# Kernel optimization log

Measured on AMD Instinct MI355X. Metric: run time of the kernel, lower is better.

Reference implementation:

```python
import jax, jax.numpy as jnp
import numpy as np

V = 6890      # SMPL vertex count
JNT = 24      # SMPL joints
NB = 10       # shape betas
PF = 207      # pose-blend features = 23*9
NJ_OUT = 19   # cocoplus joints
PARENTS = np.array([0, 0, 0, 0, 1, 2, 3, 4, 5, 6, 7, 8, 9, 9, 9, 12, 13, 14, 16, 17, 18, 19, 20, 21], dtype=np.int32)


def setup_inputs() -> dict:
    key = jax.random.key(0)
    ks = jax.random.split(key, 8)
    B = 512
    beta = jax.random.normal(ks[0], (B, NB), dtype=jnp.float32)
    theta = jax.random.normal(ks[1], (B, JNT * 3), dtype=jnp.float32)
    v_template = jax.random.normal(ks[2], (V, 3), dtype=jnp.float32)
    shapedirs = jax.random.normal(ks[3], (NB, V * 3), dtype=jnp.float32) * 0.01
    J_regressor = jax.random.uniform(ks[4], (V, JNT), dtype=jnp.float32)
    J_regressor = J_regressor / jnp.sum(J_regressor, axis=0, keepdims=True)
    posedirs = jax.random.normal(ks[5], (PF, V * 3), dtype=jnp.float32) * 0.01
    lbs_weights = jax.random.uniform(ks[6], (V, JNT), dtype=jnp.float32)
    lbs_weights = lbs_weights / jnp.sum(lbs_weights, axis=1, keepdims=True)
    joint_regressor = jax.random.uniform(ks[7], (V, NJ_OUT), dtype=jnp.float32)
    joint_regressor = joint_regressor / jnp.sum(joint_regressor, axis=0, keepdims=True)
    return {
        "beta": beta, "theta": theta, "v_template": v_template,
        "shapedirs": shapedirs, "J_regressor": J_regressor,
        "posedirs": posedirs, "lbs_weights": lbs_weights,
        "joint_regressor": joint_regressor,
    }


def batch_rodrigues(aa):
    # aa: [N,3] axis-angle -> [N,3,3] rotation via unit quaternion
    angle = jnp.linalg.norm(aa + 1e-8, axis=1, keepdims=True)  # [N,1]
    axis = aa / angle
    half = angle * 0.5
    w = jnp.cos(half)[:, 0]
    xyz = axis * jnp.sin(half)
    x, y, z = xyz[:, 0], xyz[:, 1], xyz[:, 2]
    w2, x2, y2, z2 = w * w, x * x, y * y, z * z
    wx, wy, wz = w * x, w * y, w * z
    xy, xz, yz = x * y, x * z, y * z
    R = jnp.stack([
        w2 + x2 - y2 - z2, 2 * (xy - wz), 2 * (xz + wy),
        2 * (xy + wz), w2 - x2 + y2 - z2, 2 * (yz - wx),
        2 * (xz - wy), 2 * (yz + wx), w2 - x2 - y2 + z2,
    ], axis=1).reshape(-1, 3, 3)
    return R


def _make_A(R, t):
    # R: [B,3,3], t: [B,3] -> [B,4,4]
    B = R.shape[0]
    top = jnp.concatenate([R, t[:, :, None]], axis=2)          # [B,3,4]
    bot = jnp.broadcast_to(jnp.array([0., 0., 0., 1.], R.dtype), (B, 1, 4))
    return jnp.concatenate([top, bot], axis=1)


def global_rigid_transform(Rs, J):
    # Rs: [B,24,3,3], J: [B,24,3]; kinematic-chain FK
    results = [_make_A(Rs[:, 0], J[:, 0])]
    for i in range(1, JNT):
        t = J[:, i] - J[:, PARENTS[i]]
        results.append(results[PARENTS[i]] @ _make_A(Rs[:, i], t))
    A = jnp.stack(results, axis=1)                              # [B,24,4,4]
    J_transformed = A[:, :, :3, 3]
    # remove rest-pose joint translation: A - [0 | A @ [J;0]]
    J_homo = jnp.concatenate([J, jnp.zeros_like(J[:, :, :1])], axis=2)  # [B,24,4]
    init_bone = jnp.einsum('bjpq,bjq->bjp', A, J_homo)          # [B,24,4]
    A_rel = A - jnp.concatenate(
        [jnp.zeros(A.shape[:3] + (3,), A.dtype), init_bone[..., None]], axis=-1)
    return J_transformed, A_rel


def reference(beta, theta, v_template, shapedirs, J_regressor, posedirs,
              lbs_weights, joint_regressor):
    B = beta.shape[0]
    # shape blend
    v_shaped = (beta @ shapedirs).reshape(B, V, 3) + v_template   # [B,V,3]
    # rest-pose joints
    J = jnp.einsum('bvc,vj->bjc', v_shaped, J_regressor)          # [B,24,3]
    # pose rotations
    Rs = batch_rodrigues(theta.reshape(-1, 3)).reshape(B, JNT, 3, 3)
    pose_feature = (Rs[:, 1:] - jnp.eye(3, dtype=Rs.dtype)).reshape(B, PF)
    v_posed = (pose_feature @ posedirs).reshape(B, V, 3) + v_shaped
    # FK
    _, A = global_rigid_transform(Rs, J)                          # [B,24,4,4]
    # skinning
    T = jnp.einsum('vj,bjpq->bvpq', lbs_weights, A)               # [B,V,4,4]
    v_homo = jnp.concatenate(
        [v_posed, jnp.ones((B, V, 1), v_posed.dtype)], axis=2)    # [B,V,4]
    verts = jnp.einsum('bvpq,bvq->bvp', T[:, :, :3, :], v_homo)   # [B,V,3]
    joints = jnp.einsum('bvc,vj->bjc', verts, joint_regressor)    # [B,19,3]
    return joints
```

## Files before the change

### kernel.cpp

```cpp
#include <hip/hip_runtime.h>
#include <math.h>

#define NV 6890
#define N3 20670
#define NJNT 24
#define NBETA 10
#define NPF 207
#define NJO 19
#define NBATCH 512
#define NJK 456
#define NJKP 512
#define NCOEF 218
#define PROWSP 768
#define KPAD 6912
#define KSPLIT 12
#define KCH 576
#define CSTR 224
#define CSTRV 6912

#define TR2 54
#define RODB 48
#define SJB 264
#define PMA 5913
#define PMO 27
#define PMZ 3051
#define PMT (PMA + PMO + PMZ)
#define CHB 48
#define C4R 1728
#define CMB (NJKP * C4R / 256)
#define D4R 219
#define RSP 2
#define RCH 109
#define SSTRIDE ((size_t)NBATCH * 3 * NJK)

typedef __attribute__((ext_vector_type(8))) short bfx8;
typedef __attribute__((ext_vector_type(4))) float fx4;

#define LDSP(x) ((__attribute__((address_space(3))) void*)(x))
#define GLBP(x) ((const __attribute__((address_space(1))) void*)(x))

__constant__ int d_par[NJNT] = {0,0,0,0,1,2,3,4,5,6,7,8,9,9,9,12,13,14,16,17,18,19,20,21};
__constant__ int d_path[NJNT][9] = {
  {0,-1,-1,-1,-1,-1,-1,-1,-1},
  {0,1,-1,-1,-1,-1,-1,-1,-1},
  {0,2,-1,-1,-1,-1,-1,-1,-1},
  {0,3,-1,-1,-1,-1,-1,-1,-1},
  {0,1,4,-1,-1,-1,-1,-1,-1},
  {0,2,5,-1,-1,-1,-1,-1,-1},
  {0,3,6,-1,-1,-1,-1,-1,-1},
  {0,1,4,7,-1,-1,-1,-1,-1},
  {0,2,5,8,-1,-1,-1,-1,-1},
  {0,3,6,9,-1,-1,-1,-1,-1},
  {0,1,4,7,10,-1,-1,-1,-1},
  {0,2,5,8,11,-1,-1,-1,-1},
  {0,3,6,9,12,-1,-1,-1,-1},
  {0,3,6,9,13,-1,-1,-1,-1},
  {0,3,6,9,14,-1,-1,-1,-1},
  {0,3,6,9,12,15,-1,-1,-1},
  {0,3,6,9,13,16,-1,-1,-1},
  {0,3,6,9,14,17,-1,-1,-1},
  {0,3,6,9,13,16,18,-1,-1},
  {0,3,6,9,14,17,19,-1,-1},
  {0,3,6,9,13,16,18,20,-1},
  {0,3,6,9,14,17,19,21,-1},
  {0,3,6,9,13,16,18,20,22},
  {0,3,6,9,14,17,19,21,23}};

__device__ inline short f2bf(float f) {
  union { float f; unsigned u; } x; x.f = f;
  unsigned r = (x.u + 0x7fffu + ((x.u >> 16) & 1u)) >> 16;
  return (short)r;
}

__global__ void __launch_bounds__(256) kA(const float* __restrict__ jr,
                                          const float* __restrict__ lbs,
                                          const float* __restrict__ Jreg,
                                          const float* __restrict__ sdirs,
                                          const float* __restrict__ vtmpl,
                                          const float* __restrict__ theta,
                                          const float* __restrict__ beta,
                                          const float* __restrict__ pdirs,
                                          float* __restrict__ jrT, float* __restrict__ wT,
                                          float* __restrict__ SJ, float* __restrict__ Rs,
                                          float* __restrict__ pfc,
                                          short* __restrict__ Pb) {
  __shared__ float red[4][3];
  __shared__ float tj[128 * NJO];
  __shared__ float tw[128 * NJNT];
  int bx = blockIdx.x, tid = threadIdx.x;
  if (bx < TR2) {
    int v0 = bx * 128;
    for (int i = tid; i < 128 * NJO; i += 256) {
      int g = v0 * NJO + i;
      tj[i] = (g < NV * NJO) ? jr[g] : 0.f;
    }
    for (int i = tid; i < 128 * NJNT; i += 256) {
      int g = v0 * NJNT + i;
      tw[i] = (g < NV * NJNT) ? lbs[g] : 0.f;
    }
    __syncthreads();
    for (int i = tid; i < 128 * (NJO + NJNT); i += 256) {
      int r = i >> 7, c = i & 127;
      int v = v0 + c;
      if (v >= NV) continue;
      if (r < NJO) jrT[(size_t)r * CSTRV + v] = tj[c * NJO + r];
      else         wT[(size_t)(r - NJO) * CSTRV + v] = tw[c * NJNT + (r - NJO)];
    }
  } else if (bx < TR2 + RODB) {
    int t2 = (bx - TR2) * 256 + tid;
    int b = t2 / NJNT, j = t2 - b * NJNT;
    float a0 = theta[b * 72 + j * 3 + 0];
    float a1 = theta[b * 72 + j * 3 + 1];
    float a2 = theta[b * 72 + j * 3 + 2];
    float e0 = a0 + 1e-8f, e1 = a1 + 1e-8f, e2 = a2 + 1e-8f;
    float ang = sqrtf(e0 * e0 + e1 * e1 + e2 * e2);
    float inv = 1.0f / ang;
    float h = 0.5f * ang;
    float w = cosf(h), s = sinf(h);
    float x = a0 * inv * s, y = a1 * inv * s, z = a2 * inv * s;
    float R[9];
    R[0] = w*w + x*x - y*y - z*z; R[1] = 2.f*(x*y - w*z); R[2] = 2.f*(x*z + w*y);
    R[3] = 2.f*(x*y + w*z); R[4] = w*w - x*x + y*y - z*z; R[5] = 2.f*(y*z - w*x);
    R[6] = 2.f*(x*z - w*y); R[7] = 2.f*(y*z + w*x); R[8] = w*w - x*x - y*y + z*z;
#pragma unroll
    for (int r = 0; r < 9; ++r) Rs[b * 216 + j * 9 + r] = R[r];
    if (j >= 1) {
#pragma unroll
      for (int r = 0; r < 9; ++r)
        pfc[b * CSTR + (j - 1) * 9 + r] = R[r] - ((r % 4 == 0) ? 1.0f : 0.0f);
    } else {
#pragma unroll
      for (int i = 0; i < NBETA; ++i) pfc[b * CSTR + NPF + i] = beta[b * NBETA + i];
      pfc[b * CSTR + NPF + NBETA] = 1.0f;
    }
  } else if (bx < TR2 + RODB + SJB) {
    int s = bx - TR2 - RODB;
    int j = s % NJNT, k = s / NJNT;
    const float* src = (k < NBETA) ? (sdirs + (size_t)k * N3) : vtmpl;
    float a0 = 0.f, a1 = 0.f, a2 = 0.f;
    for (int v = tid; v < NV; v += 256) {
      float w = Jreg[v * NJNT + j];
      a0 += w * src[v * 3 + 0];
      a1 += w * src[v * 3 + 1];
      a2 += w * src[v * 3 + 2];
    }
    int lane = tid & 63, wid = tid >> 6;
#pragma unroll
    for (int s2 = 1; s2 < 64; s2 <<= 1) {
      a0 += __shfl_xor(a0, s2); a1 += __shfl_xor(a1, s2); a2 += __shfl_xor(a2, s2);
    }
    if (lane == 0) { red[wid][0] = a0; red[wid][1] = a1; red[wid][2] = a2; }
    __syncthreads();
    if (tid == 0) {
      float* o = SJ + (k * NJNT + j) * 3;
      o[0] = red[0][0] + red[1][0] + red[2][0] + red[3][0];
      o[1] = red[0][1] + red[1][1] + red[2][1] + red[3][1];
      o[2] = red[0][2] + red[1][2] + red[2][2] + red[3][2];
    }
  } else {
    int s4 = bx - TR2 - RODB - SJB;
    if (s4 < PMA) {
      int s = s4 / 27, g = s4 - s * 27;
      const float* src; int base;
      if (s < 207)      { src = pdirs + (size_t)s * N3;         base = 3 * s; }
      else if (s < 217) { src = sdirs + (size_t)(s - 207) * N3; base = 621 + 3 * (s - 207); }
      else              { src = vtmpl;                           base = 651; }
      int v = g * 256 + tid;
      float x = 0.f, y = 0.f, z = 0.f;
      if (v < NV) { x = src[3 * v]; y = src[3 * v + 1]; z = src[3 * v + 2]; }
      Pb[(size_t)(base + 0) * KPAD + v] = f2bf(x);
      Pb[(size_t)(base + 1) * KPAD + v] = f2bf(y);
      Pb[(size_t)(base + 2) * KPAD + v] = f2bf(z);
    } else if (s4 < PMA + PMO) {
      int g = s4 - PMA;
      int v = g * 256 + tid;
      Pb[(size_t)654 * KPAD + v] = (v < NV) ? f2bf(1.0f) : (short)0;
    } else {
      int s = s4 - PMA - PMO;
      int row = 655 + s / 27, g = s % 27;
      Pb[(size_t)row * KPAD + g * 256 + tid] = (short)0;
    }
  }
}

__device__ inline void getJ(const float* __restrict__ SJ, const float* bb, int i,
                            float& o0, float& o1, float& o2) {
  int r = i * 3;
  float a0 = SJ[NBETA * 72 + r + 0];
  float a1 = SJ[NBETA * 72 + r + 1];
  float a2 = SJ[NBETA * 72 + r + 2];
#pragma unroll
  for (int k = 0; k < NBETA; ++k) {
    a0 += bb[k] * SJ[k * 72 + r + 0];
    a1 += bb[k] * SJ[k * 72 + r + 1];
    a2 += bb[k] * SJ[k * 72 + r + 2];
  }
  o0 = a0; o1 = a1; o2 = a2;
}

__global__ void __launch_bounds__(256) kB(const float* __restrict__ beta,
                                          const float* __restrict__ SJ,
                                          const float* __restrict__ Rs,
                                          const float* __restrict__ jrT,
                                          const float* __restrict__ wT,
                                          float* __restrict__ A,
                                          short* __restrict__ Cb) {
  int bx = blockIdx.x, tid = threadIdx.x;
  if (bx < CHB) {
    int idx = bx * 256 + tid;
    int b = idx / NJNT, j = idx - b * NJNT;
    const float* Rb = Rs + b * 216;
    float bb[NBETA];
#pragma unroll
    for (int k = 0; k < NBETA; ++k) bb[k] = beta[b * NBETA + k];
    float jp0, jp1, jp2;
    getJ(SJ, bb, 0, jp0, jp1, jp2);
    float T[12];
#pragma unroll
    for (int r = 0; r < 3; ++r) {
      T[r * 4 + 0] = Rb[r * 3 + 0];
      T[r * 4 + 1] = Rb[r * 3 + 1];
      T[r * 4 + 2] = Rb[r * 3 + 2];
    }
    T[3] = jp0; T[7] = jp1; T[11] = jp2;
    for (int d = 1; d < 9; ++d) {
      int i = d_path[j][d];
      if (i < 0) break;
      float ji0, ji1, ji2;
      getJ(SJ, bb, i, ji0, ji1, ji2);
      float t0 = ji0 - jp0, t1 = ji1 - jp1, t2 = ji2 - jp2;
      const float* R = Rb + i * 9;
      float R0 = R[0], R1 = R[1], R2 = R[2], R3 = R[3], R4 = R[4];
      float R5 = R[5], R6 = R[6], R7 = R[7], R8 = R[8];
#pragma unroll
      for (int r = 0; r < 3; ++r) {
        float a0 = T[r * 4 + 0], a1 = T[r * 4 + 1], a2 = T[r * 4 + 2];
        T[r * 4 + 0] = a0 * R0 + a1 * R3 + a2 * R6;
        T[r * 4 + 1] = a0 * R1 + a1 * R4 + a2 * R7;
        T[r * 4 + 2] = a0 * R2 + a1 * R5 + a2 * R8;
        T[r * 4 + 3] = a0 * t0 + a1 * t1 + a2 * t2 + T[r * 4 + 3];
      }
      jp0 = ji0; jp1 = ji1; jp2 = ji2;
    }
    float* Ab = A + b * 288 + j * 12;
#pragma unroll
    for (int r = 0; r < 3; ++r) {
      float o0 = T[r * 4 + 0], o1 = T[r * 4 + 1], o2 = T[r * 4 + 2];
      Ab[r * 4 + 0] = o0;
      Ab[r * 4 + 1] = o1;
      Ab[r * 4 + 2] = o2;
      Ab[r * 4 + 3] = T[r * 4 + 3] - (o0 * jp0 + o1 * jp1 + o2 * jp2);
    }
  } else {
    int idx = (bx - CHB) * 256 + tid;
    int jk = idx / C4R;
    int c4 = idx - jk * C4R;
    int v0 = c4 * 4;
    short4 o;
    if (jk < NJK) {
      int j = jk / NJNT, k = jk - j * NJNT;
      float4 a = *(const float4*)(jrT + (size_t)j * CSTRV + v0);
      float4 w = *(const float4*)(wT + (size_t)k * CSTRV + v0);
      o.x = (v0 + 0 < NV) ? f2bf(a.x * w.x) : (short)0;
      o.y = (v0 + 1 < NV) ? f2bf(a.y * w.y) : (short)0;
      o.z = (v0 + 2 < NV) ? f2bf(a.z * w.z) : (short)0;
      o.w = (v0 + 3 < NV) ? f2bf(a.w * w.w) : (short)0;
    } else {
      o.x = o.y = o.z = o.w = (short)0;
    }
    *(short4*)(Cb + (size_t)jk * KPAD + v0) = o;
  }
}

__global__ void __launch_bounds__(256) k_gemm(const short* __restrict__ Pb,
                                              const short* __restrict__ Cb,
                                              float* __restrict__ Dpart) {
  int m0 = blockIdx.x * 128;
  int n0 = blockIdx.y * 64;
  int kb0 = blockIdx.z * KCH;
  __shared__ __align__(16) short As[128 * 64];
  __shared__ __align__(16) short Bs[64 * 64];
  int t = threadIdx.x;
  int wid = t >> 6, lane = t & 63;
  int fgrp = lane >> 4;
  fx4 acc[2][4];
#pragma unroll
  for (int r2 = 0; r2 < 2; ++r2)
#pragma unroll
    for (int j = 0; j < 4; ++j)
#pragma unroll
      for (int r = 0; r < 4; ++r) acc[r2][j][r] = 0.f;

  int lrow = lane >> 3;
  int gsrc = (lane & 7) ^ lrow;
  const short* sA[4]; short* dA[4];
#pragma unroll
  for (int i = 0; i < 4; ++i) {
    int rb = wid * 8 + i * 32;
    sA[i] = Pb + (size_t)(m0 + rb + lrow) * KPAD + kb0 + gsrc * 8;
    dA[i] = As + rb * 64;
  }
  const short* sB[2]; short* dB[2];
#pragma unroll
  for (int i = 0; i < 2; ++i) {
    int rb = wid * 8 + i * 32;
    sB[i] = Cb + (size_t)(n0 + rb + lrow) * KPAD + kb0 + gsrc * 8;
    dB[i] = Bs + rb * 64;
  }

  for (int kk = 0; kk < KCH / 64; ++kk) {
#pragma unroll
    for (int i = 0; i < 4; ++i) {
      __builtin_amdgcn_global_load_lds(GLBP(sA[i]), LDSP(dA[i]), 16, 0, 0);
      sA[i] += 64;
    }
#pragma unroll
    for (int i = 0; i < 2; ++i) {
      __builtin_amdgcn_global_load_lds(GLBP(sB[i]), LDSP(dB[i]), 16, 0, 0);
      sB[i] += 64;
    }
    __syncthreads();
#pragma unroll
    for (int ks = 0; ks < 2; ++ks) {
      int ga = ks * 4 + fgrp;
#pragma unroll
      for (int r2 = 0; r2 < 2; ++r2) {
        int arow = wid * 32 + r2 * 16 + (lane & 15);
        bfx8 a = *(const bfx8*)(As + arow * 64 + (ga ^ (arow & 7)) * 8);
#pragma unroll
        for (int j = 0; j < 4; ++j) {
          int bcol = j * 16 + (lane & 15);
          bfx8 b = *(const bfx8*)(Bs + bcol * 64 + (ga ^ (bcol & 7)) * 8);
          acc[r2][j] = __builtin_amdgcn_mfma_f32_16x16x32_bf16(a, b, acc[r2][j], 0, 0, 0);
        }
      }
    }
    __syncthreads();
  }
  float* dz = Dpart + (size_t)blockIdx.z * PROWSP * NJKP;
#pragma unroll
  for (int r2 = 0; r2 < 2; ++r2) {
    float* dst = dz + (size_t)(m0 + wid * 32 + r2 * 16 + (lane >> 4) * 4) * NJKP
               + n0 + (lane & 15);
#pragma unroll
    for (int j = 0; j < 4; ++j)
#pragma unroll
      for (int r = 0; r < 4; ++r)
        dst[(size_t)r * NJKP + j * 16] = acc[r2][j][r];
  }
}

__global__ void k_redD4(const float* __restrict__ Dpart, float* __restrict__ D4) {
  int idx = blockIdx.x * 256 + threadIdx.x;
  if (idx >= D4R * NJKP) return;
  int r = idx / NJKP, jk = idx - r * NJKP;
  float4 o;
  if (r < NCOEF) {
    float s0 = 0.f, s1 = 0.f, s2 = 0.f;
#pragma unroll
    for (int z = 0; z < KSPLIT; ++z) {
      const float* dp = Dpart + (size_t)z * PROWSP * NJKP + jk;
      s0 += dp[(size_t)(3 * r + 0) * NJKP];
      s1 += dp[(size_t)(3 * r + 1) * NJKP];
      s2 += dp[(size_t)(3 * r + 2) * NJKP];
    }
    o = make_float4(s0, s1, s2, 0.f);
  } else {
    float s = 0.f;
#pragma unroll
    for (int z = 0; z < KSPLIT; ++z)
      s += Dpart[(size_t)z * PROWSP * NJKP + (size_t)654 * NJKP + jk];
    o = make_float4(s, 0.f, 0.f, 0.f);
  }
  ((float4*)D4)[idx] = o;
}

__global__ void __launch_bounds__(256) k_S5b(const float* __restrict__ D4,
                                             const float* __restrict__ pfc,
                                             float* __restrict__ Spart) {
  int n0 = blockIdx.x * 64;
  int b0 = blockIdx.y * 8;
  int r0 = blockIdx.z * RCH;
  int r1 = r0 + RCH; if (r1 > NCOEF) r1 = NCOEF;
  int tid = threadIdx.x;
  int jk = tid & 63;
  int bg = (tid >> 6) * 2;
  const float4* D4v = (const float4*)D4;
  int jkg = n0 + jk;
  const float* c0p = pfc + (size_t)(b0 + bg + 0) * CSTR;
  const float* c1p = pfc + (size_t)(b0 + bg + 1) * CSTR;
  float a00 = 0.f, a01 = 0.f, a02 = 0.f, a10 = 0.f, a11 = 0.f, a12 = 0.f;
#pragma unroll 4
  for (int r = r0; r < r1; ++r) {
    float4 d = D4v[(size_t)r * NJKP + jkg];
    float c0 = c0p[r];
    float c1 = c1p[r];
    a00 += c0 * d.x; a01 += c0 * d.y; a02 += c0 * d.z;
    a10 += c1 * d.x; a11 += c1 * d.y; a12 += c1 * d.z;
  }
  if (jkg < NJK) {
    float* base = Spart + (size_t)blockIdx.z * SSTRIDE;
    float* o0 = base + ((size_t)(b0 + bg + 0) * 3) * NJK + jkg;
    float* o1 = base + ((size_t)(b0 + bg + 1) * 3) * NJK + jkg;
    o0[0 * NJK] = a00; o0[1 * NJK] = a01; o0[2 * NJK] = a02;
    o1[0 * NJK] = a10; o1[1 * NJK] = a11; o1[2 * NJK] = a12;
  }
}

__global__ void __launch_bounds__(128) k_final3(const float* __restrict__ Spart,
                                                const float* __restrict__ D4,
                                                const float* __restrict__ A,
                                                float* __restrict__ out) {
  __shared__ float S_ls[2 * 3 * NJK];
  __shared__ float A_ls[2 * 288];
  __shared__ float c0_ls[NJK];
  int blk = blockIdx.x, tid = threadIdx.x;
  int b0 = blk * 2;
  size_t sbase = (size_t)(b0 * 3) * NJK;
  for (int i = tid; i < 2 * 3 * NJK; i += 128)
    S_ls[i] = Spart[sbase + i] + Spart[SSTRIDE + sbase + i];
  for (int i = tid; i < 2 * 288; i += 128)
    A_ls[i] = A[(size_t)b0 * 288 + i];
  for (int i = tid; i < NJK; i += 128)
    c0_ls[i] = D4[((size_t)NCOEF * NJKP + i) * 4];
  __syncthreads();
  if (tid >= 2 * NJO * 3) return;
  int bq = tid / 57, r = tid - bq * 57;
  int j = r / 3, c = r - j * 3;
  const float* S0 = S_ls + (bq * 3 + 0) * NJK + j * NJNT;
  const float* S1 = S_ls + (bq * 3 + 1) * NJK + j * NJNT;
  const float* S2 = S_ls + (bq * 3 + 2) * NJK + j * NJNT;
  const float* Ab = A_ls + bq * 288;
  const float* cc = c0_ls + j * NJNT;
  float acc = 0.f;
#pragma unroll 4
  for (int k = 0; k < NJNT; ++k) {
    const float* Ar = Ab + k * 12 + c * 4;
    acc += Ar[0] * S0[k] + Ar[1] * S1[k] + Ar[2] * S2[k] + Ar[3] * cc[k];
  }
  out[(size_t)(b0 + bq) * 57 + r] = acc;
}

extern "C" void kernel_launch(void* const* d_in, const int* in_sizes, int n_in,
                              void* d_out, int out_size, void* d_ws, size_t ws_size,
                              hipStream_t stream) {
  const float* beta  = (const float*)d_in[0];
  const float* theta = (const float*)d_in[1];
  const float* vtmpl = (const float*)d_in[2];
  const float* sdirs = (const float*)d_in[3];
  const float* Jreg  = (const float*)d_in[4];
  const float* pdirs = (const float*)d_in[5];
  const float* lbs   = (const float*)d_in[6];
  const float* jreg2 = (const float*)d_in[7];
  float* out = (float*)d_out;

  float* ws    = (float*)d_ws;
  short* Cb    = (short*)ws;
  short* Pb    = Cb + (size_t)NJKP * KPAD;
  float* Dpart = (float*)(Pb + (size_t)PROWSP * KPAD);
  float* D4    = Dpart + (size_t)KSPLIT * PROWSP * NJKP;
  float* Spart = D4    + (size_t)D4R * NJKP * 4;
  float* pfc   = Spart + (size_t)RSP * SSTRIDE;
  float* Rs    = pfc   + (size_t)NBATCH * CSTR;
  float* A     = Rs    + (size_t)NBATCH * 216;
  float* jrT   = A     + (size_t)NBATCH * 288;
  float* wT    = jrT   + (size_t)NJO * CSTRV;
  float* SJ    = wT    + (size_t)NJNT * CSTRV;

  kA<<<dim3(TR2 + RODB + SJB + PMT), 256, 0, stream>>>(
      jreg2, lbs, Jreg, sdirs, vtmpl, theta, beta, pdirs,
      jrT, wT, SJ, Rs, pfc, Pb);
  kB<<<dim3(CHB + CMB), 256, 0, stream>>>(beta, SJ, Rs, jrT, wT, A, Cb);
  k_gemm<<<dim3(PROWSP / 128, NJKP / 64, KSPLIT), 256, 0, stream>>>(Pb, Cb, Dpart);
  k_redD4<<<dim3((D4R * NJKP + 255) / 256), 256, 0, stream>>>(Dpart, D4);
  k_S5b<<<dim3(NJKP / 64, NBATCH / 8, RSP), 256, 0, stream>>>(D4, pfc, Spart);
  k_final3<<<dim3(NBATCH / 2), 128, 0, stream>>>(Spart, D4, A, out);
}
```

Measured before the change: 79.43 us.

## Rebalance setup kernels, vectorize Pb packing, move FK into reduction kernel

The packing of posedirs/shapedirs/template into bf16 now uses float4 loads and short4 stores, with one thread handling four vertices, and zero-fill is done with short4 stores. The shape-joint regression moves from kA to kB and reads a transposed J_regressor, which kA now also writes, so the accesses are coalesced. The forward-kinematics chain moves from kB into the split-K reduction kernel, since it needs SJ from kB. The GEMM K-split drops from 12 to 9 slices with larger chunks, which means less partial-sum traffic and fewer blocks. Together these rebalance work across the launches and shorten the long serial blocks.

```diff
diff --git a/kernel.cpp b/kernel.cpp
--- a/kernel.cpp
+++ b/kernel.cpp
@@ -13,21 +13,20 @@
 #define NCOEF 218
 #define PROWSP 768
 #define KPAD 6912
-#define KSPLIT 12
-#define KCH 576
+#define KSPLIT 9
+#define KCH 768
 #define CSTR 224
 #define CSTRV 6912
 
 #define TR2 54
 #define RODB 48
-#define SJB 264
-#define PMA 5913
-#define PMO 27
-#define PMZ 3051
-#define PMT (PMA + PMO + PMZ)
-#define CHB 48
+#define PMV 1479
+#define PMP 763
 #define C4R 1728
 #define CMB (NJKP * C4R / 256)
+#define SJB 264
+#define RD4B 438
+#define CHB 48
 #define D4R 219
 #define RSP 2
 #define RCH 109
@@ -81,12 +80,12 @@
                                           const float* __restrict__ beta,
                                           const float* __restrict__ pdirs,
                                           float* __restrict__ jrT, float* __restrict__ wT,
-                                          float* __restrict__ SJ, float* __restrict__ Rs,
-                                          float* __restrict__ pfc,
+                                          float* __restrict__ jgT,
+                                          float* __restrict__ Rs, float* __restrict__ pfc,
                                           short* __restrict__ Pb) {
-  __shared__ float red[4][3];
   __shared__ float tj[128 * NJO];
   __shared__ float tw[128 * NJNT];
+  __shared__ float tg[128 * NJNT];
   int bx = blockIdx.x, tid = threadIdx.x;
   if (bx < TR2) {
     int v0 = bx * 128;
@@ -97,14 +96,16 @@
     for (int i = tid; i < 128 * NJNT; i += 256) {
       int g = v0 * NJNT + i;
       tw[i] = (g < NV * NJNT) ? lbs[g] : 0.f;
+      tg[i] = (g < NV * NJNT) ? Jreg[g] : 0.f;
     }
     __syncthreads();
-    for (int i = tid; i < 128 * (NJO + NJNT); i += 256) {
+    for (int i = tid; i < 128 * (NJO + 2 * NJNT); i += 256) {
       int r = i >> 7, c = i & 127;
       int v = v0 + c;
       if (v >= NV) continue;
-      if (r < NJO) jrT[(size_t)r * CSTRV + v] = tj[c * NJO + r];
-      else         wT[(size_t)(r - NJO) * CSTRV + v] = tw[c * NJNT + (r - NJO)];
+      if (r < NJO)            jrT[(size_t)r * CSTRV + v] = tj[c * NJO + r];
+      else if (r < NJO + NJNT) wT[(size_t)(r - NJO) * CSTRV + v] = tw[c * NJNT + (r - NJO)];
+      else                    jgT[(size_t)(r - NJO - NJNT) * CSTRV + v] = tg[c * NJNT + (r - NJO - NJNT)];
     }
   } else if (bx < TR2 + RODB) {
     int t2 = (bx - TR2) * 256 + tid;
@@ -133,126 +134,66 @@
       for (int i = 0; i < NBETA; ++i) pfc[b * CSTR + NPF + i] = beta[b * NBETA + i];
       pfc[b * CSTR + NPF + NBETA] = 1.0f;
     }
-  } else if (bx < TR2 + RODB + SJB) {
-    int s = bx - TR2 - RODB;
-    int j = s % NJNT, k = s / NJNT;
-    const float* src = (k < NBETA) ? (sdirs + (size_t)k * N3) : vtmpl;
-    float a0 = 0.f, a1 = 0.f, a2 = 0.f;
-    for (int v = tid; v < NV; v += 256) {
-      float w = Jreg[v * NJNT + j];
-      a0 += w * src[v * 3 + 0];
-      a1 += w * src[v * 3 + 1];
-      a2 += w * src[v * 3 + 2];
-    }
-    int lane = tid & 63, wid = tid >> 6;
-#pragma unroll
-    for (int s2 = 1; s2 < 64; s2 <<= 1) {
-      a0 += __shfl_xor(a0, s2); a1 += __shfl_xor(a1, s2); a2 += __shfl_xor(a2, s2);
-    }
-    if (lane == 0) { red[wid][0] = a0; red[wid][1] = a1; red[wid][2] = a2; }
-    __syncthreads();
-    if (tid == 0) {
-      float* o = SJ + (k * NJNT + j) * 3;
-      o[0] = red[0][0] + red[1][0] + red[2][0] + red[3][0];
-      o[1] = red[0][1] + red[1][1] + red[2][1] + red[3][1];
-      o[2] = red[0][2] + red[1][2] + red[2][2] + red[3][2];
+  } else if (bx < TR2 + RODB + PMV) {
+    int idx = (bx - TR2 - RODB) * 256 + tid;
+    if (idx >= 219 * C4R) return;
+    int s = idx / C4R, c4 = idx - s * C4R;
+    int v0 = c4 * 4;
+    if (s == 218) {
+      short one = f2bf(1.0f);
+      short4 o;
+      o.x = (v0 + 0 < NV) ? one : (short)0;
+      o.y = (v0 + 1 < NV) ? one : (short)0;
+      o.z = (v0 + 2 < NV) ? one : (short)0;
+      o.w = (v0 + 3 < NV) ? one : (short)0;
+      *(short4*)(Pb + (size_t)654 * KPAD + v0) = o;
+      return;
+    }
+    const float* src; int base;
+    if (s < 207)      { src = pdirs + (size_t)s * N3;         base = 3 * s; }
+    else if (s < 217) { src = sdirs + (size_t)(s - 207) * N3; base = 621 + 3 * (s - 207); }
+    else              { src = vtmpl;                           base = 651; }
+    float e[12];
+    if (v0 + 4 <= NV) {
+      float4 a = *(const float4*)(src + 3 * v0);
+      float4 b = *(const float4*)(src + 3 * v0 + 4);
+      float4 c = *(const float4*)(src + 3 * v0 + 8);
+      e[0]=a.x; e[1]=a.y; e[2]=a.z; e[3]=a.w; e[4]=b.x; e[5]=b.y;
+      e[6]=b.z; e[7]=b.w; e[8]=c.x; e[9]=c.y; e[10]=c.z; e[11]=c.w;
+    } else {
+#pragma unroll
+      for (int i = 0; i < 12; ++i) {
+        int f = 3 * v0 + i;
+        e[i] = (f < N3) ? src[f] : 0.f;
+      }
+    }
+#pragma unroll
+    for (int q = 0; q < 3; ++q) {
+      short4 o;
+      o.x = f2bf(e[0 + q]); o.y = f2bf(e[3 + q]);
+      o.z = f2bf(e[6 + q]); o.w = f2bf(e[9 + q]);
+      *(short4*)(Pb + (size_t)(base + q) * KPAD + v0) = o;
     }
   } else {
-    int s4 = bx - TR2 - RODB - SJB;
-    if (s4 < PMA) {
-      int s = s4 / 27, g = s4 - s * 27;
-      const float* src; int base;
-      if (s < 207)      { src = pdirs + (size_t)s * N3;         base = 3 * s; }
-      else if (s < 217) { src = sdirs + (size_t)(s - 207) * N3; base = 621 + 3 * (s - 207); }
-      else              { src = vtmpl;                           base = 651; }
-      int v = g * 256 + tid;
-      float x = 0.f, y = 0.f, z = 0.f;
-      if (v < NV) { x = src[3 * v]; y = src[3 * v + 1]; z = src[3 * v + 2]; }
-      Pb[(size_t)(base + 0) * KPAD + v] = f2bf(x);
-      Pb[(size_t)(base + 1) * KPAD + v] = f2bf(y);
-      Pb[(size_t)(base + 2) * KPAD + v] = f2bf(z);
-    } else if (s4 < PMA + PMO) {
-      int g = s4 - PMA;
-      int v = g * 256 + tid;
-      Pb[(size_t)654 * KPAD + v] = (v < NV) ? f2bf(1.0f) : (short)0;
-    } else {
-      int s = s4 - PMA - PMO;
-      int row = 655 + s / 27, g = s % 27;
-      Pb[(size_t)row * KPAD + g * 256 + tid] = (short)0;
-    }
-  }
-}
-
-__device__ inline void getJ(const float* __restrict__ SJ, const float* bb, int i,
-                            float& o0, float& o1, float& o2) {
-  int r = i * 3;
-  float a0 = SJ[NBETA * 72 + r + 0];
-  float a1 = SJ[NBETA * 72 + r + 1];
-  float a2 = SJ[NBETA * 72 + r + 2];
-#pragma unroll
-  for (int k = 0; k < NBETA; ++k) {
-    a0 += bb[k] * SJ[k * 72 + r + 0];
-    a1 += bb[k] * SJ[k * 72 + r + 1];
-    a2 += bb[k] * SJ[k * 72 + r + 2];
-  }
-  o0 = a0; o1 = a1; o2 = a2;
-}
-
-__global__ void __launch_bounds__(256) kB(const float* __restrict__ beta,
-                                          const float* __restrict__ SJ,
-                                          const float* __restrict__ Rs,
-                                          const float* __restrict__ jrT,
+    int idx = (bx - TR2 - RODB - PMV) * 256 + tid;
+    if (idx >= 113 * C4R) return;
+    int r = idx / C4R, c4 = idx - r * C4R;
+    short4 z; z.x = z.y = z.z = z.w = (short)0;
+    *(short4*)(Pb + (size_t)(655 + r) * KPAD + c4 * 4) = z;
+  }
+}
+
+__global__ void __launch_bounds__(256) kB(const float* __restrict__ jrT,
                                           const float* __restrict__ wT,
-                                          float* __restrict__ A,
-                                          short* __restrict__ Cb) {
+                                          const float* __restrict__ jgT,
+                                          const float* __restrict__ sdirs,
+                                          const float* __restrict__ vtmpl,
+                                          short* __restrict__ Cb,
+                                          float* __restrict__ SJ) {
+  __shared__ float red[4][3];
   int bx = blockIdx.x, tid = threadIdx.x;
-  if (bx < CHB) {
+  if (bx < CMB) {
     int idx = bx * 256 + tid;
-    int b = idx / NJNT, j = idx - b * NJNT;
-    const float* Rb = Rs + b * 216;
-    float bb[NBETA];
-#pragma unroll
-    for (int k = 0; k < NBETA; ++k) bb[k] = beta[b * NBETA + k];
-    float jp0, jp1, jp2;
-    getJ(SJ, bb, 0, jp0, jp1, jp2);
-    float T[12];
-#pragma unroll
-    for (int r = 0; r < 3; ++r) {
-      T[r * 4 + 0] = Rb[r * 3 + 0];
-      T[r * 4 + 1] = Rb[r * 3 + 1];
-      T[r * 4 + 2] = Rb[r * 3 + 2];
-    }
-    T[3] = jp0; T[7] = jp1; T[11] = jp2;
-    for (int d = 1; d < 9; ++d) {
-      int i = d_path[j][d];
-      if (i < 0) break;
-      float ji0, ji1, ji2;
-      getJ(SJ, bb, i, ji0, ji1, ji2);
-      float t0 = ji0 - jp0, t1 = ji1 - jp1, t2 = ji2 - jp2;
-      const float* R = Rb + i * 9;
-      float R0 = R[0], R1 = R[1], R2 = R[2], R3 = R[3], R4 = R[4];
-      float R5 = R[5], R6 = R[6], R7 = R[7], R8 = R[8];
-#pragma unroll
-      for (int r = 0; r < 3; ++r) {
-        float a0 = T[r * 4 + 0], a1 = T[r * 4 + 1], a2 = T[r * 4 + 2];
-        T[r * 4 + 0] = a0 * R0 + a1 * R3 + a2 * R6;
-        T[r * 4 + 1] = a0 * R1 + a1 * R4 + a2 * R7;
-        T[r * 4 + 2] = a0 * R2 + a1 * R5 + a2 * R8;
-        T[r * 4 + 3] = a0 * t0 + a1 * t1 + a2 * t2 + T[r * 4 + 3];
-      }
-      jp0 = ji0; jp1 = ji1; jp2 = ji2;
-    }
-    float* Ab = A + b * 288 + j * 12;
-#pragma unroll
-    for (int r = 0; r < 3; ++r) {
-      float o0 = T[r * 4 + 0], o1 = T[r * 4 + 1], o2 = T[r * 4 + 2];
-      Ab[r * 4 + 0] = o0;
-      Ab[r * 4 + 1] = o1;
-      Ab[r * 4 + 2] = o2;
-      Ab[r * 4 + 3] = T[r * 4 + 3] - (o0 * jp0 + o1 * jp1 + o2 * jp2);
-    }
-  } else {
-    int idx = (bx - CHB) * 256 + tid;
     int jk = idx / C4R;
     int c4 = idx - jk * C4R;
     int v0 = c4 * 4;
@@ -269,6 +210,31 @@
       o.x = o.y = o.z = o.w = (short)0;
     }
     *(short4*)(Cb + (size_t)jk * KPAD + v0) = o;
+  } else {
+    int s = bx - CMB;
+    int j = s % NJNT, k = s / NJNT;
+    const float* src = (k < NBETA) ? (sdirs + (size_t)k * N3) : vtmpl;
+    const float* jg = jgT + (size_t)j * CSTRV;
+    float a0 = 0.f, a1 = 0.f, a2 = 0.f;
+    for (int v = tid; v < NV; v += 256) {
+      float w = jg[v];
+      a0 += w * src[v * 3 + 0];
+      a1 += w * src[v * 3 + 1];
+      a2 += w * src[v * 3 + 2];
+    }
+    int lane = tid & 63, wid = tid >> 6;
+#pragma unroll
+    for (int s2 = 1; s2 < 64; s2 <<= 1) {
+      a0 += __shfl_xor(a0, s2); a1 += __shfl_xor(a1, s2); a2 += __shfl_xor(a2, s2);
+    }
+    if (lane == 0) { red[wid][0] = a0; red[wid][1] = a1; red[wid][2] = a2; }
+    __syncthreads();
+    if (tid == 0) {
+      float* o = SJ + (k * NJNT + j) * 3;
+      o[0] = red[0][0] + red[1][0] + red[2][0] + red[3][0];
+      o[1] = red[0][1] + red[1][1] + red[2][1] + red[3][1];
+      o[2] = red[0][2] + red[1][2] + red[2][2] + red[3][2];
+    }
   }
 }
 
@@ -350,29 +316,96 @@
   }
 }
 
-__global__ void k_redD4(const float* __restrict__ Dpart, float* __restrict__ D4) {
-  int idx = blockIdx.x * 256 + threadIdx.x;
-  if (idx >= D4R * NJKP) return;
-  int r = idx / NJKP, jk = idx - r * NJKP;
-  float4 o;
-  if (r < NCOEF) {
-    float s0 = 0.f, s1 = 0.f, s2 = 0.f;
-#pragma unroll
-    for (int z = 0; z < KSPLIT; ++z) {
-      const float* dp = Dpart + (size_t)z * PROWSP * NJKP + jk;
-      s0 += dp[(size_t)(3 * r + 0) * NJKP];
-      s1 += dp[(size_t)(3 * r + 1) * NJKP];
-      s2 += dp[(size_t)(3 * r + 2) * NJKP];
-    }
-    o = make_float4(s0, s1, s2, 0.f);
+__device__ inline void getJ(const float* __restrict__ SJ, const float* bb, int i,
+                            float& o0, float& o1, float& o2) {
+  int r = i * 3;
+  float a0 = SJ[NBETA * 72 + r + 0];
+  float a1 = SJ[NBETA * 72 + r + 1];
+  float a2 = SJ[NBETA * 72 + r + 2];
+#pragma unroll
+  for (int k = 0; k < NBETA; ++k) {
+    a0 += bb[k] * SJ[k * 72 + r + 0];
+    a1 += bb[k] * SJ[k * 72 + r + 1];
+    a2 += bb[k] * SJ[k * 72 + r + 2];
+  }
+  o0 = a0; o1 = a1; o2 = a2;
+}
+
+__global__ void __launch_bounds__(256) k_redD4C(const float* __restrict__ Dpart,
+                                                const float* __restrict__ beta,
+                                                const float* __restrict__ SJ,
+                                                const float* __restrict__ Rs,
+                                                float* __restrict__ D4,
+                                                float* __restrict__ A) {
+  int bx = blockIdx.x, tid = threadIdx.x;
+  if (bx < RD4B) {
+    int idx = bx * 256 + tid;
+    int r = idx / NJKP, jk = idx - r * NJKP;
+    float4 o;
+    if (r < NCOEF) {
+      float s0 = 0.f, s1 = 0.f, s2 = 0.f;
+#pragma unroll
+      for (int z = 0; z < KSPLIT; ++z) {
+        const float* dp = Dpart + (size_t)z * PROWSP * NJKP + jk;
+        s0 += dp[(size_t)(3 * r + 0) * NJKP];
+        s1 += dp[(size_t)(3 * r + 1) * NJKP];
+        s2 += dp[(size_t)(3 * r + 2) * NJKP];
+      }
+      o = make_float4(s0, s1, s2, 0.f);
+    } else {
+      float s = 0.f;
+#pragma unroll
+      for (int z = 0; z < KSPLIT; ++z)
+        s += Dpart[(size_t)z * PROWSP * NJKP + (size_t)654 * NJKP + jk];
+      o = make_float4(s, 0.f, 0.f, 0.f);
+    }
+    ((float4*)D4)[idx] = o;
   } else {
-    float s = 0.f;
-#pragma unroll
-    for (int z = 0; z < KSPLIT; ++z)
-      s += Dpart[(size_t)z * PROWSP * NJKP + (size_t)654 * NJKP + jk];
-    o = make_float4(s, 0.f, 0.f, 0.f);
-  }
-  ((float4*)D4)[idx] = o;
+    int idx = (bx - RD4B) * 256 + tid;
+    int b = idx / NJNT, j = idx - b * NJNT;
+    const float* Rb = Rs + b * 216;
+    float bb[NBETA];
+#pragma unroll
+    for (int k = 0; k < NBETA; ++k) bb[k] = beta[b * NBETA + k];
+    float jp0, jp1, jp2;
+    getJ(SJ, bb, 0, jp0, jp1, jp2);
+    float T[12];
+#pragma unroll
+    for (int r = 0; r < 3; ++r) {
+      T[r * 4 + 0] = Rb[r * 3 + 0];
+      T[r * 4 + 1] = Rb[r * 3 + 1];
+      T[r * 4 + 2] = Rb[r * 3 + 2];
+    }
+    T[3] = jp0; T[7] = jp1; T[11] = jp2;
+    for (int d = 1; d < 9; ++d) {
+      int i = d_path[j][d];
+      if (i < 0) break;
+      float ji0, ji1, ji2;
+      getJ(SJ, bb, i, ji0, ji1, ji2);
+      float t0 = ji0 - jp0, t1 = ji1 - jp1, t2 = ji2 - jp2;
+      const float* R = Rb + i * 9;
+      float R0 = R[0], R1 = R[1], R2 = R[2], R3 = R[3], R4 = R[4];
+      float R5 = R[5], R6 = R[6], R7 = R[7], R8 = R[8];
+#pragma unroll
+      for (int r = 0; r < 3; ++r) {
+        float a0 = T[r * 4 + 0], a1 = T[r * 4 + 1], a2 = T[r * 4 + 2];
+        T[r * 4 + 0] = a0 * R0 + a1 * R3 + a2 * R6;
+        T[r * 4 + 1] = a0 * R1 + a1 * R4 + a2 * R7;
+        T[r * 4 + 2] = a0 * R2 + a1 * R5 + a2 * R8;
+        T[r * 4 + 3] = a0 * t0 + a1 * t1 + a2 * t2 + T[r * 4 + 3];
+      }
+      jp0 = ji0; jp1 = ji1; jp2 = ji2;
+    }
+    float* Ab = A + b * 288 + j * 12;
+#pragma unroll
+    for (int r = 0; r < 3; ++r) {
+      float o0 = T[r * 4 + 0], o1 = T[r * 4 + 1], o2 = T[r * 4 + 2];
+      Ab[r * 4 + 0] = o0;
+      Ab[r * 4 + 1] = o1;
+      Ab[r * 4 + 2] = o2;
+      Ab[r * 4 + 3] = T[r * 4 + 3] - (o0 * jp0 + o1 * jp1 + o2 * jp2);
+    }
+  }
 }
 
 __global__ void __launch_bounds__(256) k_S5b(const float* __restrict__ D4,
@@ -465,14 +498,15 @@
   float* A     = Rs    + (size_t)NBATCH * 216;
   float* jrT   = A     + (size_t)NBATCH * 288;
   float* wT    = jrT   + (size_t)NJO * CSTRV;
-  float* SJ    = wT    + (size_t)NJNT * CSTRV;
-
-  kA<<<dim3(TR2 + RODB + SJB + PMT), 256, 0, stream>>>(
+  float* jgT   = wT    + (size_t)NJNT * CSTRV;
+  float* SJ    = jgT   + (size_t)NJNT * CSTRV;
+
+  kA<<<dim3(TR2 + RODB + PMV + PMP), 256, 0, stream>>>(
       jreg2, lbs, Jreg, sdirs, vtmpl, theta, beta, pdirs,
-      jrT, wT, SJ, Rs, pfc, Pb);
-  kB<<<dim3(CHB + CMB), 256, 0, stream>>>(beta, SJ, Rs, jrT, wT, A, Cb);
+      jrT, wT, jgT, Rs, pfc, Pb);
+  kB<<<dim3(CMB + SJB), 256, 0, stream>>>(jrT, wT, jgT, sdirs, vtmpl, Cb, SJ);
   k_gemm<<<dim3(PROWSP / 128, NJKP / 64, KSPLIT), 256, 0, stream>>>(Pb, Cb, Dpart);
-  k_redD4<<<dim3((D4R * NJKP + 255) / 256), 256, 0, stream>>>(Dpart, D4);
+  k_redD4C<<<dim3(RD4B + CHB), 256, 0, stream>>>(Dpart, beta, SJ, Rs, D4, A);
   k_S5b<<<dim3(NJKP / 64, NBATCH / 8, RSP), 256, 0, stream>>>(D4, pfc, Spart);
   k_final3<<<dim3(NBATCH / 2), 128, 0, stream>>>(Spart, D4, A, out);
 }
```

Measured after the change: 88.66 us. 11.6% more time.
